# Kernel tuning notes

Measured on AMD Instinct MI355X. Metric: run time of the kernel, lower is better.

The kernel has to match this reference:

```python
import jax, jax.numpy as jnp
import numpy as np

B, D, H, E, K = 16384, 4096, 2048, 64, 2
TEMPERATURE = 0.8  # training=True


def setup_inputs() -> dict:
    key = jax.random.key(0)
    k1, k2, k3 = jax.random.split(key, 3)
    x = jax.random.normal(k1, (B, D), dtype=jnp.float32)
    W1 = jax.random.normal(k2, (H, D), dtype=jnp.float32) * 0.02
    b1 = jnp.zeros((H,), dtype=jnp.float32)
    W2 = jax.random.normal(k3, (E, H), dtype=jnp.float32) * 0.02
    b2 = jnp.zeros((E,), dtype=jnp.float32)
    return {"x": x, "W1": W1, "b1": b1, "W2": W2, "b2": b2}


def reference(x, W1, b1, W2, b2):
    # router MLP: Linear(D->H) -> ReLU -> Linear(H->E)
    h = jax.nn.relu(jnp.einsum('bd,hd->bh', x, W1) + b1)
    router_logits = jnp.einsum('bh,eh->be', h, W2) + b2  # [B, E]

    # temperature-scaled softmax for routing
    routing_probs = jax.nn.softmax(router_logits / TEMPERATURE, axis=1)
    routing_weights, expert_indices = jax.lax.top_k(routing_probs, K)  # [B, K]
    routing_weights = routing_weights / routing_weights.sum(axis=1, keepdims=True)

    # entropy-based uncertainty uses UN-scaled logits
    full_probs = jax.nn.softmax(router_logits, axis=1)
    entropy = -jnp.sum(full_probs * jnp.log(full_probs + 1e-10), axis=1).mean()
    uncertainty = entropy / jnp.log(jnp.float32(E))
    return routing_weights, expert_indices, uncertainty
```

## Files before the change

kernel.cpp:

```cpp
#include <hip/hip_runtime.h>
#include <hip/hip_bf16.h>
#include <math.h>

#define B_ROWS 16384
#define D_DIM  4096
#define H_DIM  2048
#define E_DIM  64
#define TEMP   0.8f

typedef __bf16 bf16x8 __attribute__((ext_vector_type(8)));
typedef float  f32x4  __attribute__((ext_vector_type(4)));
typedef unsigned short ushort8 __attribute__((ext_vector_type(8)));

__device__ __forceinline__ unsigned short bf_rne(float f) {
  unsigned u = __float_as_uint(f);
  u += 0x7FFF + ((u >> 16) & 1);
  return (unsigned short)(u >> 16);
}

__device__ __forceinline__ void async_copy16(const void* g, void* l) {
  __builtin_amdgcn_global_load_lds(
      (const __attribute__((address_space(1))) void*)g,
      (__attribute__((address_space(3))) void*)l, 16, 0, 0);
}

__global__ __launch_bounds__(256) void split_kernel(
    const float* __restrict__ in, unsigned short* __restrict__ hi,
    unsigned short* __restrict__ lo) {
  const size_t i = ((size_t)blockIdx.x * 256 + threadIdx.x) * 8;
  float4 v0 = *(const float4*)(in + i);
  float4 v1 = *(const float4*)(in + i + 4);
  float f[8] = {v0.x, v0.y, v0.z, v0.w, v1.x, v1.y, v1.z, v1.w};
  ushort8 hv, lv;
#pragma unroll
  for (int j = 0; j < 8; ++j) {
    unsigned short h = bf_rne(f[j]);
    float fh = __uint_as_float(((unsigned)h) << 16);
    hv[j] = h;
    lv[j] = bf_rne(f[j] - fh);
  }
  *(ushort8*)(hi + i) = hv;
  *(ushort8*)(lo + i) = lv;
}

#define BM 128
#define BN 128
#define BKK 32

__global__ __launch_bounds__(256) void gemm1_mfma_kernel(
    const float* __restrict__ x,
    const unsigned short* __restrict__ w1h,
    const unsigned short* __restrict__ w1l,
    const float* __restrict__ b1, float* __restrict__ Hout) {
  __shared__ unsigned short Ah[BM * BKK];
  __shared__ unsigned short Al[BM * BKK];
  __shared__ unsigned short Bh[BN * BKK];
  __shared__ unsigned short Bl[BN * BKK];

  const int t    = threadIdx.x;
  const int lane = t & 63;
  const int w    = t >> 6;
  const int wm   = w >> 1;
  const int wn   = w & 1;
  const int m0   = blockIdx.y * BM;
  const int n0   = blockIdx.x * BN;

  const int e0 = (w * 2 + 0) * 512 + lane * 8;
  const int e1 = (w * 2 + 1) * 512 + lane * 8;
  const int r0 = e0 >> 5, c0 = e0 & 31;
  const int r1 = e1 >> 5, c1 = e1 & 31;
  const unsigned short* bh_g0 = w1h + (size_t)(n0 + r0) * D_DIM + c0;
  const unsigned short* bh_g1 = w1h + (size_t)(n0 + r1) * D_DIM + c1;
  const unsigned short* bl_g0 = w1l + (size_t)(n0 + r0) * D_DIM + c0;
  const unsigned short* bl_g1 = w1l + (size_t)(n0 + r1) * D_DIM + c1;
  unsigned short* bh_l0 = &Bh[e0];
  unsigned short* bh_l1 = &Bh[e1];
  unsigned short* bl_l0 = &Bl[e0];
  unsigned short* bl_l1 = &Bl[e1];

  const int ar = t >> 1;
  const int ac = (t & 1) * 16;
  const float* xp = x + (size_t)(m0 + ar) * D_DIM + ac;
  unsigned short* ah_w = &Ah[ar * BKK + ac];
  unsigned short* al_w = &Al[ar * BKK + ac];

  const int koff = (lane >> 4) * 8;
  const unsigned short* a_rd[4];
  const unsigned short* b_rd[4];
#pragma unroll
  for (int f = 0; f < 4; ++f) {
    a_rd[f] = &Ah[(wm * 64 + f * 16 + (lane & 15)) * BKK + koff];
    b_rd[f] = &Bh[(wn * 64 + f * 16 + (lane & 15)) * BKK + koff];
  }
  const int lo_off_a = (int)(Al - Ah);
  const int lo_off_b = (int)(Bl - Bh);

  f32x4 acc[4][4];
#pragma unroll
  for (int i = 0; i < 4; ++i)
#pragma unroll
    for (int j = 0; j < 4; ++j) acc[i][j] = (f32x4)0.f;

  for (int k0 = 0; k0 < D_DIM; k0 += BKK) {
    async_copy16(bh_g0 + k0, bh_l0);
    async_copy16(bh_g1 + k0, bh_l1);
    async_copy16(bl_g0 + k0, bl_l0);
    async_copy16(bl_g1 + k0, bl_l1);

    float4 v[4];
#pragma unroll
    for (int j = 0; j < 4; ++j) v[j] = *(const float4*)(xp + k0 + j * 4);
    float f[16] = {v[0].x, v[0].y, v[0].z, v[0].w, v[1].x, v[1].y, v[1].z, v[1].w,
                   v[2].x, v[2].y, v[2].z, v[2].w, v[3].x, v[3].y, v[3].z, v[3].w};
    ushort8 hv0, hv1, lv0, lv1;
#pragma unroll
    for (int j = 0; j < 8; ++j) {
      unsigned short h = bf_rne(f[j]);
      float fh = __uint_as_float(((unsigned)h) << 16);
      hv0[j] = h;
      lv0[j] = bf_rne(f[j] - fh);
    }
#pragma unroll
    for (int j = 0; j < 8; ++j) {
      unsigned short h = bf_rne(f[8 + j]);
      float fh = __uint_as_float(((unsigned)h) << 16);
      hv1[j] = h;
      lv1[j] = bf_rne(f[8 + j] - fh);
    }
    *(ushort8*)(ah_w)     = hv0;
    *(ushort8*)(ah_w + 8) = hv1;
    *(ushort8*)(al_w)     = lv0;
    *(ushort8*)(al_w + 8) = lv1;

    __syncthreads();

    bf16x8 fa_h[4], fa_l[4], fb_h[4], fb_l[4];
#pragma unroll
    for (int ff = 0; ff < 4; ++ff) {
      fa_h[ff] = *(const bf16x8*)(a_rd[ff]);
      fa_l[ff] = *(const bf16x8*)(a_rd[ff] + lo_off_a);
      fb_h[ff] = *(const bf16x8*)(b_rd[ff]);
      fb_l[ff] = *(const bf16x8*)(b_rd[ff] + lo_off_b);
    }
#pragma unroll
    for (int i = 0; i < 4; ++i)
#pragma unroll
      for (int j = 0; j < 4; ++j) {
        acc[i][j] = __builtin_amdgcn_mfma_f32_16x16x32_bf16(fa_h[i], fb_h[j], acc[i][j], 0, 0, 0);
        acc[i][j] = __builtin_amdgcn_mfma_f32_16x16x32_bf16(fa_l[i], fb_h[j], acc[i][j], 0, 0, 0);
        acc[i][j] = __builtin_amdgcn_mfma_f32_16x16x32_bf16(fa_h[i], fb_l[j], acc[i][j], 0, 0, 0);
      }
    __syncthreads();
  }

#pragma unroll
  for (int fn = 0; fn < 4; ++fn) {
    const int n = n0 + wn * 64 + fn * 16 + (lane & 15);
    const float bias = b1[n];
#pragma unroll
    for (int fm = 0; fm < 4; ++fm) {
      const int mbase = m0 + wm * 64 + fm * 16 + (lane >> 4) * 4;
#pragma unroll
      for (int r = 0; r < 4; ++r) {
        float vv = acc[fm][fn][r] + bias;
        Hout[(size_t)(mbase + r) * H_DIM + n] = fmaxf(vv, 0.f);
      }
    }
  }
}

#define F_BM 64
#define F_BK 32

__global__ __launch_bounds__(256) void gemm2_router_kernel(
    const float* __restrict__ h,
    const unsigned short* __restrict__ w2h,
    const unsigned short* __restrict__ w2l,
    const float* __restrict__ b2,
    float* __restrict__ out, float* __restrict__ accum) {
  __shared__ unsigned short Ah[F_BM * F_BK];
  __shared__ unsigned short Al[F_BM * F_BK];
  __shared__ unsigned short Bh[E_DIM * F_BK];
  __shared__ unsigned short Bl[E_DIM * F_BK];
  __shared__ float LG[F_BM][E_DIM + 1];

  const int t    = threadIdx.x;
  const int lane = t & 63;
  const int w    = t >> 6;
  const int m0   = blockIdx.x * F_BM;

  const int ar = t >> 2;
  const int ac = (t & 3) * 8;
  const float* hp = h + (size_t)(m0 + ar) * H_DIM + ac;
  unsigned short* ah_w = &Ah[ar * F_BK + ac];
  unsigned short* al_w = &Al[ar * F_BK + ac];

  const unsigned short* bh_g = w2h + (size_t)ar * H_DIM + ac;
  const unsigned short* bl_g = w2l + (size_t)ar * H_DIM + ac;
  unsigned short* bh_l = &Bh[t * 8];
  unsigned short* bl_l = &Bl[t * 8];

  const int koff = (lane >> 4) * 8;
  const unsigned short* a_rd = &Ah[(w * 16 + (lane & 15)) * F_BK + koff];
  const unsigned short* b_rd[4];
#pragma unroll
  for (int f = 0; f < 4; ++f)
    b_rd[f] = &Bh[(f * 16 + (lane & 15)) * F_BK + koff];
  const int lo_off_a = (int)(Al - Ah);
  const int lo_off_b = (int)(Bl - Bh);

  f32x4 acc[4];
#pragma unroll
  for (int f = 0; f < 4; ++f) acc[f] = (f32x4)0.f;

  for (int k0 = 0; k0 < H_DIM; k0 += F_BK) {
    async_copy16(bh_g + k0, bh_l);
    async_copy16(bl_g + k0, bl_l);

    float4 v0 = *(const float4*)(hp + k0);
    float4 v1 = *(const float4*)(hp + k0 + 4);
    float f[8] = {v0.x, v0.y, v0.z, v0.w, v1.x, v1.y, v1.z, v1.w};
    ushort8 hv, lv;
#pragma unroll
    for (int j = 0; j < 8; ++j) {
      unsigned short hh = bf_rne(f[j]);
      float fh = __uint_as_float(((unsigned)hh) << 16);
      hv[j] = hh;
      lv[j] = bf_rne(f[j] - fh);
    }
    *(ushort8*)ah_w = hv;
    *(ushort8*)al_w = lv;

    __syncthreads();

    bf16x8 fa_h = *(const bf16x8*)(a_rd);
    bf16x8 fa_l = *(const bf16x8*)(a_rd + lo_off_a);
#pragma unroll
    for (int f = 0; f < 4; ++f) {
      bf16x8 fb_h = *(const bf16x8*)(b_rd[f]);
      bf16x8 fb_l = *(const bf16x8*)(b_rd[f] + lo_off_b);
      acc[f] = __builtin_amdgcn_mfma_f32_16x16x32_bf16(fa_h, fb_h, acc[f], 0, 0, 0);
      acc[f] = __builtin_amdgcn_mfma_f32_16x16x32_bf16(fa_l, fb_h, acc[f], 0, 0, 0);
      acc[f] = __builtin_amdgcn_mfma_f32_16x16x32_bf16(fa_h, fb_l, acc[f], 0, 0, 0);
    }
    __syncthreads();
  }

#pragma unroll
  for (int f = 0; f < 4; ++f) {
    const int e = f * 16 + (lane & 15);
    const float bias = b2[e];
#pragma unroll
    for (int r = 0; r < 4; ++r) {
      const int ml = w * 16 + (lane >> 4) * 4 + r;
      LG[ml][e] = acc[f][r] + bias;
    }
  }
  __syncthreads();

  if (t < F_BM) {
    const int row = m0 + t;
    float l0 = LG[t][0]; int i0 = 0;
    float l1 = -INFINITY; int i1 = -1;
#pragma unroll
    for (int e = 1; e < E_DIM; ++e) {
      float v = LG[t][e];
      if (v > l0)      { l1 = l0; i1 = i0; l0 = v; i0 = e; }
      else if (v > l1) { l1 = v; i1 = e; }
    }

    const float eT = expf((l1 - l0) / TEMP);
    const float w0 = 1.f / (1.f + eT);
    const float w1 = eT / (1.f + eT);

    float Z = 0.f;
#pragma unroll
    for (int e = 0; e < E_DIM; ++e) Z += expf(LG[t][e] - l0);
    const float invZ = 1.f / Z;
    float ent = 0.f;
#pragma unroll
    for (int e = 0; e < E_DIM; ++e) {
      float p = expf(LG[t][e] - l0) * invZ;
      ent -= p * logf(p + 1e-10f);
    }

    out[(size_t)row * 2 + 0] = w0;
    out[(size_t)row * 2 + 1] = w1;
    out[(size_t)B_ROWS * 2 + (size_t)row * 2 + 0] = (float)i0;
    out[(size_t)B_ROWS * 2 + (size_t)row * 2 + 1] = (float)i1;

#pragma unroll
    for (int off = 32; off > 0; off >>= 1) ent += __shfl_down(ent, off);
    if (t == 0) atomicAdd(accum, ent);
  }
}

__global__ void zero_kernel(float* p) { p[0] = 0.f; }

__global__ void finalize_kernel(const float* __restrict__ accum,
                                float* __restrict__ out) {
  out[(size_t)B_ROWS * 4] = accum[0] / ((float)B_ROWS * logf((float)E_DIM));
}

extern "C" void kernel_launch(void* const* d_in, const int* in_sizes, int n_in,
                              void* d_out, int out_size, void* d_ws,
                              size_t ws_size, hipStream_t stream) {
  const float* x  = (const float*)d_in[0];
  const float* W1 = (const float*)d_in[1];
  const float* b1 = (const float*)d_in[2];
  const float* W2 = (const float*)d_in[3];
  const float* b2 = (const float*)d_in[4];
  float* out = (float*)d_out;

  unsigned short* w1h = (unsigned short*)d_ws;
  unsigned short* w1l = w1h + (size_t)H_DIM * D_DIM;
  unsigned short* w2h = w1l + (size_t)H_DIM * D_DIM;
  unsigned short* w2l = w2h + (size_t)E_DIM * H_DIM;
  float* h     = (float*)(w2l + (size_t)E_DIM * H_DIM);
  float* accum = h + (size_t)B_ROWS * H_DIM;

  zero_kernel<<<1, 1, 0, stream>>>(accum);

  split_kernel<<<(H_DIM * D_DIM) / (256 * 8), 256, 0, stream>>>(W1, w1h, w1l);
  split_kernel<<<(E_DIM * H_DIM) / (256 * 8), 256, 0, stream>>>(W2, w2h, w2l);

  dim3 g1(H_DIM / BN, B_ROWS / BM);
  gemm1_mfma_kernel<<<g1, 256, 0, stream>>>(x, w1h, w1l, b1, h);

  gemm2_router_kernel<<<B_ROWS / F_BM, 256, 0, stream>>>(h, w2h, w2l, b2, out, accum);

  finalize_kernel<<<1, 1, 0, stream>>>(accum, out);
}
```

Baseline: 1.279 ms.

## Pre-split activations to bf16 hi/lo and load GEMM tiles via async LDS copies

Adds a pre-pass that splits x into bf16 hi/lo planes so GEMM1 can stage both operands with async global-to-LDS copies using an XOR-swizzled layout, instead of converting fp32 x inside the main loop. GEMM1 now writes the hidden activations as bf16 hi/lo pairs, so GEMM2 also loads them asynchronously, and GEMM2 moves to a larger K tile with a matching swizzle. The aim is to cut per-iteration conversion work and LDS bank conflicts. The cost is an extra full pass over x plus a large workspace requirement, with a fallback path when the workspace is too small.

```diff
diff --git a/kernel.cpp b/kernel.cpp
--- a/kernel.cpp
+++ b/kernel.cpp
@@ -47,11 +47,124 @@
 #define BN 128
 #define BKK 32
 
-__global__ __launch_bounds__(256) void gemm1_mfma_kernel(
+__global__ __launch_bounds__(256) void gemm1_async_kernel(
+    const unsigned short* __restrict__ xh, const unsigned short* __restrict__ xl,
+    const unsigned short* __restrict__ w1h, const unsigned short* __restrict__ w1l,
+    const float* __restrict__ b1,
+    unsigned short* __restrict__ hhp, unsigned short* __restrict__ hlp) {
+  __shared__ unsigned short Ah[BM * BKK];
+  __shared__ unsigned short Al[BM * BKK];
+  __shared__ unsigned short Bh[BN * BKK];
+  __shared__ unsigned short Bl[BN * BKK];
+
+  const int t    = threadIdx.x;
+  const int lane = t & 63;
+  const int w    = t >> 6;
+  const int wm   = w >> 1;
+  const int wn   = w & 1;
+  const int m0   = blockIdx.y * BM;
+  const int n0   = blockIdx.x * BN;
+
+  const unsigned short* sAh[2];
+  const unsigned short* sAl[2];
+  const unsigned short* sBh[2];
+  const unsigned short* sBl[2];
+  unsigned short* dAh[2];
+  unsigned short* dAl[2];
+  unsigned short* dBh[2];
+  unsigned short* dBl[2];
+#pragma unroll
+  for (int c = 0; c < 2; ++c) {
+    const int chunk = c * 4 + w;
+    const int row   = chunk * 16 + (lane >> 2);
+    const int col   = ((lane & 3) * 8) ^ (((row >> 1) & 3) << 3);
+    const int p     = chunk * 512 + lane * 8;
+    sAh[c] = xh  + (size_t)(m0 + row) * D_DIM + col;
+    sAl[c] = xl  + (size_t)(m0 + row) * D_DIM + col;
+    sBh[c] = w1h + (size_t)(n0 + row) * D_DIM + col;
+    sBl[c] = w1l + (size_t)(n0 + row) * D_DIM + col;
+    dAh[c] = &Ah[p];
+    dAl[c] = &Al[p];
+    dBh[c] = &Bh[p];
+    dBl[c] = &Bl[p];
+  }
+
+  const int koff = (lane >> 4) * 8;
+  const unsigned short* a_rd[4];
+  const unsigned short* b_rd[4];
+#pragma unroll
+  for (int f = 0; f < 4; ++f) {
+    const int Ra = wm * 64 + f * 16 + (lane & 15);
+    const int ca = koff ^ (((Ra >> 1) & 3) << 3);
+    a_rd[f] = &Ah[Ra * BKK + ca];
+    const int Rb = wn * 64 + f * 16 + (lane & 15);
+    const int cb = koff ^ (((Rb >> 1) & 3) << 3);
+    b_rd[f] = &Bh[Rb * BKK + cb];
+  }
+  const int lo_off_a = (int)(Al - Ah);
+  const int lo_off_b = (int)(Bl - Bh);
+
+  f32x4 acc[4][4];
+#pragma unroll
+  for (int i = 0; i < 4; ++i)
+#pragma unroll
+    for (int j = 0; j < 4; ++j) acc[i][j] = (f32x4)0.f;
+
+  for (int k0 = 0; k0 < D_DIM; k0 += BKK) {
+#pragma unroll
+    for (int c = 0; c < 2; ++c) {
+      async_copy16(sAh[c] + k0, dAh[c]);
+      async_copy16(sAl[c] + k0, dAl[c]);
+      async_copy16(sBh[c] + k0, dBh[c]);
+      async_copy16(sBl[c] + k0, dBl[c]);
+    }
+    __syncthreads();
+
+    bf16x8 fa_h[4], fa_l[4], fb_h[4], fb_l[4];
+#pragma unroll
+    for (int ff = 0; ff < 4; ++ff) {
+      fa_h[ff] = *(const bf16x8*)(a_rd[ff]);
+      fa_l[ff] = *(const bf16x8*)(a_rd[ff] + lo_off_a);
+      fb_h[ff] = *(const bf16x8*)(b_rd[ff]);
+      fb_l[ff] = *(const bf16x8*)(b_rd[ff] + lo_off_b);
+    }
+#pragma unroll
+    for (int i = 0; i < 4; ++i)
+#pragma unroll
+      for (int j = 0; j < 4; ++j) {
+        acc[i][j] = __builtin_amdgcn_mfma_f32_16x16x32_bf16(fa_h[i], fb_h[j], acc[i][j], 0, 0, 0);
+        acc[i][j] = __builtin_amdgcn_mfma_f32_16x16x32_bf16(fa_l[i], fb_h[j], acc[i][j], 0, 0, 0);
+        acc[i][j] = __builtin_amdgcn_mfma_f32_16x16x32_bf16(fa_h[i], fb_l[j], acc[i][j], 0, 0, 0);
+      }
+    __syncthreads();
+  }
+
+#pragma unroll
+  for (int fn = 0; fn < 4; ++fn) {
+    const int n = n0 + wn * 64 + fn * 16 + (lane & 15);
+    const float bias = b1[n];
+#pragma unroll
+    for (int fm = 0; fm < 4; ++fm) {
+      const int mbase = m0 + wm * 64 + fm * 16 + (lane >> 4) * 4;
+#pragma unroll
+      for (int r = 0; r < 4; ++r) {
+        const float vv = fmaxf(acc[fm][fn][r] + bias, 0.f);
+        const unsigned short hv = bf_rne(vv);
+        const float fh = __uint_as_float(((unsigned)hv) << 16);
+        const unsigned short lv = bf_rne(vv - fh);
+        hhp[(size_t)(mbase + r) * H_DIM + n] = hv;
+        hlp[(size_t)(mbase + r) * H_DIM + n] = lv;
+      }
+    }
+  }
+}
+
+__global__ __launch_bounds__(256) void gemm1_fb_kernel(
     const float* __restrict__ x,
     const unsigned short* __restrict__ w1h,
     const unsigned short* __restrict__ w1l,
-    const float* __restrict__ b1, float* __restrict__ Hout) {
+    const float* __restrict__ b1,
+    unsigned short* __restrict__ hhp, unsigned short* __restrict__ hlp) {
   __shared__ unsigned short Ah[BM * BKK];
   __shared__ unsigned short Al[BM * BKK];
   __shared__ unsigned short Bh[BN * BKK];
@@ -162,18 +275,23 @@
       const int mbase = m0 + wm * 64 + fm * 16 + (lane >> 4) * 4;
 #pragma unroll
       for (int r = 0; r < 4; ++r) {
-        float vv = acc[fm][fn][r] + bias;
-        Hout[(size_t)(mbase + r) * H_DIM + n] = fmaxf(vv, 0.f);
+        const float vv = fmaxf(acc[fm][fn][r] + bias, 0.f);
+        const unsigned short hv = bf_rne(vv);
+        const float fh = __uint_as_float(((unsigned)hv) << 16);
+        const unsigned short lv = bf_rne(vv - fh);
+        hhp[(size_t)(mbase + r) * H_DIM + n] = hv;
+        hlp[(size_t)(mbase + r) * H_DIM + n] = lv;
       }
     }
   }
 }
 
 #define F_BM 64
-#define F_BK 32
+#define F_BK 64
 
 __global__ __launch_bounds__(256) void gemm2_router_kernel(
-    const float* __restrict__ h,
+    const unsigned short* __restrict__ hhp,
+    const unsigned short* __restrict__ hlp,
     const unsigned short* __restrict__ w2h,
     const unsigned short* __restrict__ w2l,
     const float* __restrict__ b2,
@@ -189,23 +307,45 @@
   const int w    = t >> 6;
   const int m0   = blockIdx.x * F_BM;
 
-  const int ar = t >> 2;
-  const int ac = (t & 3) * 8;
-  const float* hp = h + (size_t)(m0 + ar) * H_DIM + ac;
-  unsigned short* ah_w = &Ah[ar * F_BK + ac];
-  unsigned short* al_w = &Al[ar * F_BK + ac];
-
-  const unsigned short* bh_g = w2h + (size_t)ar * H_DIM + ac;
-  const unsigned short* bl_g = w2l + (size_t)ar * H_DIM + ac;
-  unsigned short* bh_l = &Bh[t * 8];
-  unsigned short* bl_l = &Bl[t * 8];
+  const unsigned short* sAh[2];
+  const unsigned short* sAl[2];
+  const unsigned short* sBh[2];
+  const unsigned short* sBl[2];
+  unsigned short* dAh[2];
+  unsigned short* dAl[2];
+  unsigned short* dBh[2];
+  unsigned short* dBl[2];
+#pragma unroll
+  for (int c = 0; c < 2; ++c) {
+    const int chunk = c * 4 + w;
+    const int row   = chunk * 8 + (lane >> 3);
+    const int col   = ((lane & 7) * 8) ^ ((row & 7) << 3);
+    const int p     = chunk * 512 + lane * 8;
+    sAh[c] = hhp + (size_t)(m0 + row) * H_DIM + col;
+    sAl[c] = hlp + (size_t)(m0 + row) * H_DIM + col;
+    sBh[c] = w2h + (size_t)row * H_DIM + col;
+    sBl[c] = w2l + (size_t)row * H_DIM + col;
+    dAh[c] = &Ah[p];
+    dAl[c] = &Al[p];
+    dBh[c] = &Bh[p];
+    dBl[c] = &Bl[p];
+  }
 
   const int koff = (lane >> 4) * 8;
-  const unsigned short* a_rd = &Ah[(w * 16 + (lane & 15)) * F_BK + koff];
-  const unsigned short* b_rd[4];
-#pragma unroll
-  for (int f = 0; f < 4; ++f)
-    b_rd[f] = &Bh[(f * 16 + (lane & 15)) * F_BK + koff];
+  const int Ra = w * 16 + (lane & 15);
+  const unsigned short* a_rd[2];
+  const unsigned short* b_rd[2][4];
+#pragma unroll
+  for (int kk = 0; kk < 2; ++kk) {
+    const int ca = (kk * 32 + koff) ^ ((Ra & 7) << 3);
+    a_rd[kk] = &Ah[Ra * F_BK + ca];
+#pragma unroll
+    for (int f = 0; f < 4; ++f) {
+      const int Rb = f * 16 + (lane & 15);
+      const int cb = (kk * 32 + koff) ^ ((Rb & 7) << 3);
+      b_rd[kk][f] = &Bh[Rb * F_BK + cb];
+    }
+  }
   const int lo_off_a = (int)(Al - Ah);
   const int lo_off_b = (int)(Bl - Bh);
 
@@ -214,34 +354,27 @@
   for (int f = 0; f < 4; ++f) acc[f] = (f32x4)0.f;
 
   for (int k0 = 0; k0 < H_DIM; k0 += F_BK) {
-    async_copy16(bh_g + k0, bh_l);
-    async_copy16(bl_g + k0, bl_l);
-
-    float4 v0 = *(const float4*)(hp + k0);
-    float4 v1 = *(const float4*)(hp + k0 + 4);
-    float f[8] = {v0.x, v0.y, v0.z, v0.w, v1.x, v1.y, v1.z, v1.w};
-    ushort8 hv, lv;
-#pragma unroll
-    for (int j = 0; j < 8; ++j) {
-      unsigned short hh = bf_rne(f[j]);
-      float fh = __uint_as_float(((unsigned)hh) << 16);
-      hv[j] = hh;
-      lv[j] = bf_rne(f[j] - fh);
-    }
-    *(ushort8*)ah_w = hv;
-    *(ushort8*)al_w = lv;
-
-    __syncthreads();
-
-    bf16x8 fa_h = *(const bf16x8*)(a_rd);
-    bf16x8 fa_l = *(const bf16x8*)(a_rd + lo_off_a);
-#pragma unroll
-    for (int f = 0; f < 4; ++f) {
-      bf16x8 fb_h = *(const bf16x8*)(b_rd[f]);
-      bf16x8 fb_l = *(const bf16x8*)(b_rd[f] + lo_off_b);
-      acc[f] = __builtin_amdgcn_mfma_f32_16x16x32_bf16(fa_h, fb_h, acc[f], 0, 0, 0);
-      acc[f] = __builtin_amdgcn_mfma_f32_16x16x32_bf16(fa_l, fb_h, acc[f], 0, 0, 0);
-      acc[f] = __builtin_amdgcn_mfma_f32_16x16x32_bf16(fa_h, fb_l, acc[f], 0, 0, 0);
+#pragma unroll
+    for (int c = 0; c < 2; ++c) {
+      async_copy16(sAh[c] + k0, dAh[c]);
+      async_copy16(sAl[c] + k0, dAl[c]);
+      async_copy16(sBh[c] + k0, dBh[c]);
+      async_copy16(sBl[c] + k0, dBl[c]);
+    }
+    __syncthreads();
+
+#pragma unroll
+    for (int kk = 0; kk < 2; ++kk) {
+      bf16x8 fa_h = *(const bf16x8*)(a_rd[kk]);
+      bf16x8 fa_l = *(const bf16x8*)(a_rd[kk] + lo_off_a);
+#pragma unroll
+      for (int f = 0; f < 4; ++f) {
+        bf16x8 fb_h = *(const bf16x8*)(b_rd[kk][f]);
+        bf16x8 fb_l = *(const bf16x8*)(b_rd[kk][f] + lo_off_b);
+        acc[f] = __builtin_amdgcn_mfma_f32_16x16x32_bf16(fa_h, fb_h, acc[f], 0, 0, 0);
+        acc[f] = __builtin_amdgcn_mfma_f32_16x16x32_bf16(fa_l, fb_h, acc[f], 0, 0, 0);
+        acc[f] = __builtin_amdgcn_mfma_f32_16x16x32_bf16(fa_h, fb_l, acc[f], 0, 0, 0);
+      }
     }
     __syncthreads();
   }
@@ -312,22 +445,38 @@
   const float* b2 = (const float*)d_in[4];
   float* out = (float*)d_out;
 
+  const size_t SZ_W1 = (size_t)H_DIM * D_DIM;
+  const size_t SZ_W2 = (size_t)E_DIM * H_DIM;
+  const size_t SZ_H  = (size_t)B_ROWS * H_DIM;
+  const size_t SZ_X  = (size_t)B_ROWS * D_DIM;
+
   unsigned short* w1h = (unsigned short*)d_ws;
-  unsigned short* w1l = w1h + (size_t)H_DIM * D_DIM;
-  unsigned short* w2h = w1l + (size_t)H_DIM * D_DIM;
-  unsigned short* w2l = w2h + (size_t)E_DIM * H_DIM;
-  float* h     = (float*)(w2l + (size_t)E_DIM * H_DIM);
-  float* accum = h + (size_t)B_ROWS * H_DIM;
+  unsigned short* w1l = w1h + SZ_W1;
+  unsigned short* w2h = w1l + SZ_W1;
+  unsigned short* w2l = w2h + SZ_W2;
+  unsigned short* hhp = w2l + SZ_W2;
+  unsigned short* hlp = hhp + SZ_H;
+  float* accum        = (float*)(hlp + SZ_H);
+  unsigned short* xh  = (unsigned short*)(accum + 64);
+  unsigned short* xl  = xh + SZ_X;
+  const size_t need_bytes = (size_t)((char*)(xl + SZ_X) - (char*)d_ws);
+  const bool fast = ws_size >= need_bytes;
 
   zero_kernel<<<1, 1, 0, stream>>>(accum);
 
-  split_kernel<<<(H_DIM * D_DIM) / (256 * 8), 256, 0, stream>>>(W1, w1h, w1l);
-  split_kernel<<<(E_DIM * H_DIM) / (256 * 8), 256, 0, stream>>>(W2, w2h, w2l);
+  split_kernel<<<(int)(SZ_W1 / (256 * 8)), 256, 0, stream>>>(W1, w1h, w1l);
+  split_kernel<<<(int)(SZ_W2 / (256 * 8)), 256, 0, stream>>>(W2, w2h, w2l);
 
   dim3 g1(H_DIM / BN, B_ROWS / BM);
-  gemm1_mfma_kernel<<<g1, 256, 0, stream>>>(x, w1h, w1l, b1, h);
-
-  gemm2_router_kernel<<<B_ROWS / F_BM, 256, 0, stream>>>(h, w2h, w2l, b2, out, accum);
+  if (fast) {
+    split_kernel<<<(int)(SZ_X / (256 * 8)), 256, 0, stream>>>(x, xh, xl);
+    gemm1_async_kernel<<<g1, 256, 0, stream>>>(xh, xl, w1h, w1l, b1, hhp, hlp);
+  } else {
+    gemm1_fb_kernel<<<g1, 256, 0, stream>>>(x, w1h, w1l, b1, hhp, hlp);
+  }
+
+  gemm2_router_kernel<<<B_ROWS / F_BM, 256, 0, stream>>>(hhp, hlp, w2h, w2l, b2,
+                                                         out, accum);
 
   finalize_kernel<<<1, 1, 0, stream>>>(accum, out);
 }
```

Measured after the change: 1.308 ms. 1.02x slower.
